# Performance work log

Hardware: AMD Instinct MI355X
Metric: run time of the kernel (lower is better)

Reference implementation:

```python
import jax, jax.numpy as jnp
import numpy as np

P = 8      # input_path_dim
D = 64     # cde_state_dim
W = 16     # signature_window_size
OUT = 32   # output_path_dim
II, JJ = np.triu_indices(P, k=1)   # Lyndon words of length 2: (i, j) with i < j
L = P + II.shape[0]                # logsig size at depth 2 = 8 + 28 = 36


def lipswish(x):
    return 0.909 * jax.nn.silu(x)


def setup_inputs() -> dict:
    key = jax.random.key(0)
    ks = jax.random.split(key, 16)
    s = lambda *sh: 1.0 / np.sqrt(sh[-1])
    inp = {
        "control_values": jax.random.normal(ks[0], (32, 257, P), dtype=jnp.float32),
        # initial-condition MLP: P -> 128 -> 128 -> D, lipswish activations
        "ic_w1": jax.random.normal(ks[1], (128, P)) * s(128, P),
        "ic_b1": jnp.zeros((128,)),
        "ic_w2": jax.random.normal(ks[2], (128, 128)) * s(128, 128),
        "ic_b2": jnp.zeros((128,)),
        "ic_w3": jax.random.normal(ks[3], (D, 128)) * s(D, 128),
        "ic_b3": jnp.zeros((D,)),
        # vector-field MLP: D -> 128 -> 128 -> P*D, lipswish, final tanh
        "vf_w1": jax.random.normal(ks[4], (128, D)) * s(128, D),
        "vf_b1": jnp.zeros((128,)),
        "vf_w2": jax.random.normal(ks[5], (128, 128)) * s(128, 128),
        "vf_b2": jnp.zeros((128,)),
        "vf_w3": jax.random.normal(ks[6], (P * D, 128)) * s(P * D, 128),
        "vf_b3": jnp.zeros((P * D,)),
        # readout: D -> OUT
        "ro_w": jax.random.normal(ks[7], (OUT, D)) * s(OUT, D),
        "ro_b": jnp.zeros((OUT,)),
    }
    return {k: v.astype(jnp.float32) for k, v in inp.items()}


def _windowed_logsigs(x):
    """Depth-2 Lyndon log-signatures of piecewise-linear path x: (length, P) -> (n_windows, L)."""
    dx = jnp.diff(x, axis=0).reshape(-1, W, P)          # (nw, W, P) increments
    lev1 = dx.sum(axis=1)                               # (nw, P)
    pre = jnp.cumsum(dx, axis=1) - dx                   # X_k - X_0 within window
    s = jnp.einsum("wki,wkj->wij", pre, dx)             # iterated-integral cross terms
    area = 0.5 * (s - jnp.swapaxes(s, 1, 2))            # Levy area, antisymmetric
    lev2 = area[:, II, JJ]                              # Lyndon coords i<j: (nw, P*(P-1)/2)
    return jnp.concatenate([lev1, lev2], axis=1)        # (nw, L)


def reference(control_values, ic_w1, ic_b1, ic_w2, ic_b2, ic_w3, ic_b3,
              vf_w1, vf_b1, vf_w2, vf_b2, vf_w3, vf_b3, ro_w, ro_b):
    def ic_mlp(x):
        h = lipswish(ic_w1 @ x + ic_b1)
        h = lipswish(ic_w2 @ h + ic_b2)
        return ic_w3 @ h + ic_b3

    def vf(y):  # all P vector fields stacked: (P, D)
        h = lipswish(vf_w1 @ y + vf_b1)
        h = lipswish(vf_w2 @ h + vf_b2)
        return jnp.tanh(vf_w3 @ h + vf_b3).reshape(P, D)

    def vf_matrix(y):
        # Euclidean manifold: retract / project_to_tangent are identity.
        F = vf(y)                        # (P, D)  level-1 columns f_i(y)
        J = jax.jacfwd(vf)(y)            # (P, D, D) Jacobians df_a/dy
        M = jnp.einsum("ade,be->abd", J, F)     # M[a,b] = J_a @ f_b
        lev2 = M[JJ, II] - M[II, JJ]     # [f_i, f_j](y) = Jf_j f_i - Jf_i f_j
        return jnp.concatenate([F, lev2], axis=0).T  # (D, L)

    def solve_one(x):  # x: (length, P)
        logsigs = _windowed_logsigs(x)   # (nw, L)
        y0 = ic_mlp(x[0])
        def step(y, v):                  # one RK4 step per window (log-ODE)
            g = lambda z: vf_matrix(z) @ v
            k1 = g(y); k2 = g(y + 0.5 * k1); k3 = g(y + 0.5 * k2); k4 = g(y + k3)
            y2 = y + (k1 + 2.0 * k2 + 2.0 * k3 + k4) / 6.0
            return y2, y2
        _, ys = jax.lax.scan(step, y0, logsigs)
        hidden = jnp.concatenate([y0[None], ys], axis=0)   # (nw+1, D) evolving output
        return hidden @ ro_w.T + ro_b                      # readout, identity retract

    return jax.vmap(solve_one)(control_values)             # (B, nw+1, OUT)
```

## Files before the change

### kernel.cpp

```cpp
#include <hip/hip_runtime.h>
#include <math.h>

#define NT 1024

#define D_YCUR 0
#define D_KACC 64
#define D_T3   128
#define D_VSIG 640
#define D_HID  1216
#define D_X0   2304
#define D_TOTAL 2312

#define F_YB 0
#define F_H1 96
#define F_D1 256
#define F_H2 384
#define F_D2 544
#define F_FB 672
#define F_WM 1184
#define F_U1 1696
#define F_U2 2976
#define F_CM 4256
#define F_TOTAL 4320

static __device__ __forceinline__ double lipswish_d(double z, double* d) {
    double s = 1.0 / (1.0 + exp(-z));
    *d = 0.909 * s * (1.0 + z * (1.0 - s));
    return 0.909 * z * s;
}
static __device__ __forceinline__ float lipswish_f(float z, float* d) {
    float s = 1.0f / (1.0f + expf(-z));
    *d = 0.909f * s * (1.0f + z * (1.0f - s));
    return 0.909f * z * s;
}

template<int CTRL>
static __device__ __forceinline__ float dpp_mov_f(float v) {
    int xx = __builtin_amdgcn_update_dpp(0, __float_as_int(v), CTRL, 0xF, 0xF, false);
    return __int_as_float(xx);
}
static __device__ __forceinline__ float red8f(float v) {
    v += dpp_mov_f<0xB1>(v);
    v += dpp_mov_f<0x4E>(v);
    v += dpp_mov_f<0x141>(v);
    return v;
}
static __device__ __forceinline__ float red16f(float v) {
    v += dpp_mov_f<0xB1>(v);
    v += dpp_mov_f<0x4E>(v);
    v += dpp_mov_f<0x141>(v);
    v += dpp_mov_f<0x128>(v);
    return v;
}
static __device__ __forceinline__ float red4f(float v) {
    v += dpp_mov_f<0xB1>(v);
    v += dpp_mov_f<0x4E>(v);
    return v;
}
static __device__ __forceinline__ float red2f(float v) {
    return v + dpp_mov_f<0xB1>(v);
}

extern "C" __global__ void __launch_bounds__(NT, 1)
ncde_solve(const float* __restrict__ x,
           const float* __restrict__ ic_w1, const float* __restrict__ ic_b1,
           const float* __restrict__ ic_w2, const float* __restrict__ ic_b2,
           const float* __restrict__ ic_w3, const float* __restrict__ ic_b3,
           const float* __restrict__ vf_w1, const float* __restrict__ vf_b1,
           const float* __restrict__ vf_w2, const float* __restrict__ vf_b2,
           const float* __restrict__ vf_w3, const float* __restrict__ vf_b3,
           const float* __restrict__ ro_w,  const float* __restrict__ ro_b,
           float* __restrict__ out)
{
    __shared__ double smd[D_TOTAL];
    __shared__ __align__(16) float smf[F_TOTAL];

    const int t = threadIdx.x;
    const int b = blockIdx.x;
    const float* xb = x + (size_t)b * (257 * 8);

    const int o8 = t >> 3, p8 = t & 7;
    const int o16 = t >> 4, p16 = t & 15;
    const int m = t >> 2, q = t & 3;
    const int aT = t >> 7;

    float w1f[8];
    {
        const float4* s4 = reinterpret_cast<const float4*>(vf_w1 + o8 * 64 + 8 * p8);
        float4 v0 = s4[0], v1 = s4[1];
        w1f[0] = v0.x; w1f[1] = v0.y; w1f[2] = v0.z; w1f[3] = v0.w;
        w1f[4] = v1.x; w1f[5] = v1.y; w1f[6] = v1.z; w1f[7] = v1.w;
    }
    float w2f[16];
    {
        const float4* s4 = reinterpret_cast<const float4*>(vf_w2 + o8 * 128 + 16 * p8);
        #pragma unroll
        for (int jj = 0; jj < 4; ++jj) {
            float4 v = s4[jj];
            w2f[4 * jj] = v.x; w2f[4 * jj + 1] = v.y;
            w2f[4 * jj + 2] = v.z; w2f[4 * jj + 3] = v.w;
        }
    }
    float w1u[2][4];
    {
        float4 a = *reinterpret_cast<const float4*>(vf_w1 + o16 * 64 + 4 * p16);
        float4 c = *reinterpret_cast<const float4*>(vf_w1 + (o16 + 64) * 64 + 4 * p16);
        w1u[0][0] = a.x; w1u[0][1] = a.y; w1u[0][2] = a.z; w1u[0][3] = a.w;
        w1u[1][0] = c.x; w1u[1][1] = c.y; w1u[1][2] = c.z; w1u[1][3] = c.w;
    }
    float w2u[2][8];
    {
        const float4* sa = reinterpret_cast<const float4*>(vf_w2 + o16 * 128 + 8 * p16);
        const float4* sb = reinterpret_cast<const float4*>(vf_w2 + (o16 + 64) * 128 + 8 * p16);
        float4 a0 = sa[0], a1 = sa[1], c0 = sb[0], c1 = sb[1];
        w2u[0][0] = a0.x; w2u[0][1] = a0.y; w2u[0][2] = a0.z; w2u[0][3] = a0.w;
        w2u[0][4] = a1.x; w2u[0][5] = a1.y; w2u[0][6] = a1.z; w2u[0][7] = a1.w;
        w2u[1][0] = c0.x; w2u[1][1] = c0.y; w2u[1][2] = c0.z; w2u[1][3] = c0.w;
        w2u[1][4] = c1.x; w2u[1][5] = c1.y; w2u[1][6] = c1.z; w2u[1][7] = c1.w;
    }
    float w3a[32], w3b[32];
    {
        const float4* sa = reinterpret_cast<const float4*>(vf_w3 + (size_t)(2 * m) * 128 + 32 * q);
        const float4* sb = reinterpret_cast<const float4*>(vf_w3 + (size_t)(2 * m + 1) * 128 + 32 * q);
        #pragma unroll
        for (int jj = 0; jj < 8; ++jj) {
            float4 va = sa[jj], vb = sb[jj];
            w3a[4 * jj] = va.x; w3a[4 * jj + 1] = va.y; w3a[4 * jj + 2] = va.z; w3a[4 * jj + 3] = va.w;
            w3b[4 * jj] = vb.x; w3b[4 * jj + 1] = vb.y; w3b[4 * jj + 2] = vb.z; w3b[4 * jj + 3] = vb.w;
        }
    }
    const float b1o = vf_b1[o8];
    const float b2o = vf_b2[o8];
    const float b3a = vf_b3[2 * m];
    const float b3b = vf_b3[2 * m + 1];

    if (t < 8) smd[D_X0 + t] = (double)xb[t];
    if (t < 16) {
        const float* xr = xb + t * 16 * 8;
        double cum[8], area[28], prev[8];
        #pragma unroll
        for (int i = 0; i < 8; ++i) { cum[i] = 0.0; prev[i] = (double)xr[i]; }
        #pragma unroll
        for (int u = 0; u < 28; ++u) area[u] = 0.0;
        for (int k = 1; k <= 16; ++k) {
            double dx[8];
            #pragma unroll
            for (int i = 0; i < 8; ++i) {
                double c = (double)xr[k * 8 + i];
                dx[i] = c - prev[i];
                prev[i] = c;
            }
            #pragma unroll
            for (int i = 0; i < 7; ++i) {
                #pragma unroll
                for (int j = i + 1; j < 8; ++j) {
                    int u = 7 * i - (i * (i - 1)) / 2 + (j - i - 1);
                    area[u] += 0.5 * (cum[i] * dx[j] - cum[j] * dx[i]);
                }
            }
            #pragma unroll
            for (int i = 0; i < 8; ++i) cum[i] += dx[i];
        }
        #pragma unroll
        for (int i = 0; i < 8; ++i) smd[D_VSIG + t * 36 + i] = cum[i];
        #pragma unroll
        for (int u = 0; u < 28; ++u) smd[D_VSIG + t * 36 + 8 + u] = area[u];
    }
    __syncthreads();

    if (t < 128) {
        double acc = (double)ic_b1[t];
        #pragma unroll
        for (int e = 0; e < 8; ++e) acc += (double)ic_w1[t * 8 + e] * smd[D_X0 + e];
        double d;
        smd[D_T3 + t] = lipswish_d(acc, &d);
    }
    __syncthreads();
    if (t < 128) {
        const float4* wr = reinterpret_cast<const float4*>(ic_w2 + t * 128);
        double a0 = 0.0, a1 = 0.0, a2 = 0.0, a3 = 0.0;
        #pragma unroll
        for (int k = 0; k < 32; ++k) {
            float4 wv = wr[k];
            double2 h0 = *reinterpret_cast<const double2*>(&smd[D_T3 + 4 * k]);
            double2 h1 = *reinterpret_cast<const double2*>(&smd[D_T3 + 4 * k + 2]);
            a0 += (double)wv.x * h0.x; a1 += (double)wv.y * h0.y;
            a2 += (double)wv.z * h1.x; a3 += (double)wv.w * h1.y;
        }
        double d;
        smd[D_T3 + 128 + t] = lipswish_d((double)ic_b2[t] + (a0 + a2) + (a1 + a3), &d);
    }
    __syncthreads();
    if (t < 64) {
        const float4* wr = reinterpret_cast<const float4*>(ic_w3 + t * 128);
        double a0 = 0.0, a1 = 0.0, a2 = 0.0, a3 = 0.0;
        #pragma unroll
        for (int k = 0; k < 32; ++k) {
            float4 wv = wr[k];
            double2 h0 = *reinterpret_cast<const double2*>(&smd[D_T3 + 128 + 4 * k]);
            double2 h1 = *reinterpret_cast<const double2*>(&smd[D_T3 + 128 + 4 * k + 2]);
            a0 += (double)wv.x * h0.x; a1 += (double)wv.y * h0.y;
            a2 += (double)wv.z * h1.x; a3 += (double)wv.w * h1.y;
        }
        double y0 = (double)ic_b3[t] + (a0 + a2) + (a1 + a3);
        smd[D_YCUR + t] = y0;
        smd[D_HID + t]  = y0;
        smf[F_YB + t + 4 * (t >> 3)] = (float)y0;
        int a = t >> 3, bb = t & 7;
        double cv = 0.0;
        if (a != bb) {
            int i = a < bb ? a : bb;
            int j = a < bb ? bb : a;
            int pidx = 7 * i - (i * (i - 1)) / 2 + (j - i - 1);
            double vv = smd[D_VSIG + 8 + pidx];
            cv = (a > bb) ? vv : -vv;
        }
        smf[F_CM + t] = (float)cv;
    }
    __syncthreads();

    for (int w = 0; w < 16; ++w) {
        for (int stage = 0; stage < 4; ++stage) {
            {
                float4 y0 = *reinterpret_cast<const float4*>(&smf[F_YB + 12 * p8]);
                float4 y1 = *reinterpret_cast<const float4*>(&smf[F_YB + 12 * p8 + 4]);
                float acc = w1f[0] * y0.x + w1f[1] * y0.y + w1f[2] * y0.z + w1f[3] * y0.w
                          + w1f[4] * y1.x + w1f[5] * y1.y + w1f[6] * y1.z + w1f[7] * y1.w;
                acc = red8f(acc);
                if (p8 == 0) {
                    float d;
                    smf[F_H1 + o8 + 4 * (o8 >> 4)] = lipswish_f(acc + b1o, &d);
                    smf[F_D1 + o8] = d;
                }
            }
            __syncthreads();
            {
                const float4* hv = reinterpret_cast<const float4*>(&smf[F_H1 + 20 * p8]);
                float4 h0 = hv[0], h1 = hv[1], h2 = hv[2], h3 = hv[3];
                float a0 = w2f[0] * h0.x + w2f[1] * h0.y + w2f[2] * h0.z + w2f[3] * h0.w
                         + w2f[4] * h1.x + w2f[5] * h1.y + w2f[6] * h1.z + w2f[7] * h1.w;
                float a1 = w2f[8] * h2.x + w2f[9] * h2.y + w2f[10] * h2.z + w2f[11] * h2.w
                         + w2f[12] * h3.x + w2f[13] * h3.y + w2f[14] * h3.z + w2f[15] * h3.w;
                float acc = red8f(a0 + a1);
                if (p8 == 0) {
                    float d;
                    smf[F_H2 + o8 + 4 * (o8 >> 4)] = lipswish_f(acc + b2o, &d);
                    smf[F_D2 + o8] = d;
                }
            }
            __syncthreads();
            float F0 = 0.0f, F1 = 0.0f;
            {
                float a0 = 0.0f, a1 = 0.0f;
                #pragma unroll
                for (int jj = 0; jj < 8; ++jj) {
                    float4 hv = *reinterpret_cast<const float4*>(
                        &smf[F_H2 + 40 * q + 4 * jj + 4 * (jj >> 2)]);
                    a0 += w3a[4 * jj] * hv.x + w3a[4 * jj + 1] * hv.y
                        + w3a[4 * jj + 2] * hv.z + w3a[4 * jj + 3] * hv.w;
                    a1 += w3b[4 * jj] * hv.x + w3b[4 * jj + 1] * hv.y
                        + w3b[4 * jj + 2] * hv.z + w3b[4 * jj + 3] * hv.w;
                }
                a0 = red4f(a0);
                a1 = red4f(a1);
                if (q == 0) {
                    F0 = tanhf(a0 + b3a);
                    F1 = tanhf(a1 + b3b);
                    float2 fv; fv.x = F0; fv.y = F1;
                    *reinterpret_cast<float2*>(&smf[F_FB + 2 * m]) = fv;
                }
            }
            __syncthreads();
            if (t < 128) {
                int a = t >> 4, eq = t & 15;
                float cm[8];
                #pragma unroll
                for (int bb = 0; bb < 8; ++bb) cm[bb] = smf[F_CM + a * 8 + bb];
                float4 s; s.x = 0.0f; s.y = 0.0f; s.z = 0.0f; s.w = 0.0f;
                #pragma unroll
                for (int bb = 0; bb < 8; ++bb) {
                    float4 fv = *reinterpret_cast<const float4*>(&smf[F_FB + bb * 64 + 4 * eq]);
                    s.x += cm[bb] * fv.x; s.y += cm[bb] * fv.y;
                    s.z += cm[bb] * fv.z; s.w += cm[bb] * fv.w;
                }
                *reinterpret_cast<float4*>(&smf[F_WM + a * 64 + 4 * eq]) = s;
            }
            __syncthreads();
            {
                float d1a = smf[F_D1 + o16], d1b = smf[F_D1 + o16 + 64];
                int ob = F_U1 + o16 + 4 * (o16 >> 4);
                #pragma unroll
                for (int half = 0; half < 2; ++half) {
                    float a0[4], a1[4];
                    #pragma unroll
                    for (int ai = 0; ai < 4; ++ai) {
                        int a = 4 * half + ai;
                        float4 mv = *reinterpret_cast<const float4*>(&smf[F_WM + a * 64 + 4 * p16]);
                        a0[ai] = w1u[0][0] * mv.x + w1u[0][1] * mv.y + w1u[0][2] * mv.z + w1u[0][3] * mv.w;
                        a1[ai] = w1u[1][0] * mv.x + w1u[1][1] * mv.y + w1u[1][2] * mv.z + w1u[1][3] * mv.w;
                    }
                    #pragma unroll
                    for (int ai = 0; ai < 4; ++ai) {
                        a0[ai] = red16f(a0[ai]);
                        a1[ai] = red16f(a1[ai]);
                    }
                    if (p16 == 0) {
                        #pragma unroll
                        for (int ai = 0; ai < 4; ++ai) {
                            int a = 4 * half + ai;
                            smf[ob + a * 160]      = a0[ai] * d1a;
                            smf[ob + a * 160 + 80] = a1[ai] * d1b;
                        }
                    }
                }
            }
            __syncthreads();
            {
                float d2a = smf[F_D2 + o16], d2b = smf[F_D2 + o16 + 64];
                int ib = 8 * p16 + 4 * (p16 >> 1);
                int ob = F_U2 + o16 + 4 * (o16 >> 4);
                #pragma unroll
                for (int half = 0; half < 2; ++half) {
                    float a0[4], a1[4];
                    #pragma unroll
                    for (int ai = 0; ai < 4; ++ai) {
                        int a = 4 * half + ai;
                        float4 u0 = *reinterpret_cast<const float4*>(&smf[F_U1 + a * 160 + ib]);
                        float4 u1 = *reinterpret_cast<const float4*>(&smf[F_U1 + a * 160 + ib + 4]);
                        a0[ai] = w2u[0][0] * u0.x + w2u[0][1] * u0.y + w2u[0][2] * u0.z + w2u[0][3] * u0.w
                               + w2u[0][4] * u1.x + w2u[0][5] * u1.y + w2u[0][6] * u1.z + w2u[0][7] * u1.w;
                        a1[ai] = w2u[1][0] * u0.x + w2u[1][1] * u0.y + w2u[1][2] * u0.z + w2u[1][3] * u0.w
                               + w2u[1][4] * u1.x + w2u[1][5] * u1.y + w2u[1][6] * u1.z + w2u[1][7] * u1.w;
                    }
                    #pragma unroll
                    for (int ai = 0; ai < 4; ++ai) {
                        a0[ai] = red16f(a0[ai]);
                        a1[ai] = red16f(a1[ai]);
                    }
                    if (p16 == 0) {
                        #pragma unroll
                        for (int ai = 0; ai < 4; ++ai) {
                            int a = 4 * half + ai;
                            smf[ob + a * 160]      = a0[ai] * d2a;
                            smf[ob + a * 160 + 80] = a1[ai] * d2b;
                        }
                    }
                }
            }
            __syncthreads();
            {
                float a0 = 0.0f, a1 = 0.0f;
                #pragma unroll
                for (int jj = 0; jj < 8; ++jj) {
                    float4 uv = *reinterpret_cast<const float4*>(
                        &smf[F_U2 + aT * 160 + 40 * q + 4 * jj + 4 * (jj >> 2)]);
                    a0 += w3a[4 * jj] * uv.x + w3a[4 * jj + 1] * uv.y
                        + w3a[4 * jj + 2] * uv.z + w3a[4 * jj + 3] * uv.w;
                    a1 += w3b[4 * jj] * uv.x + w3b[4 * jj + 1] * uv.y
                        + w3b[4 * jj + 2] * uv.z + w3b[4 * jj + 3] * uv.w;
                }
                a0 = red4f(a0);
                a1 = red4f(a1);
                if (q == 0) {
                    double va = smd[D_VSIG + w * 36 + aT];
                    double2 tv;
                    tv.x = va * (double)F0 + (1.0 - (double)F0 * F0) * (double)a0;
                    tv.y = va * (double)F1 + (1.0 - (double)F1 * F1) * (double)a1;
                    *reinterpret_cast<double2*>(&smd[D_T3 + 2 * m]) = tv;
                }
            }
            __syncthreads();
            if (t < 64) {
                double g = 0.0;
                #pragma unroll
                for (int a = 0; a < 8; ++a) g += smd[D_T3 + a * 64 + t];
                double y = smd[D_YCUR + t];
                int yp = F_YB + t + 4 * (t >> 3);
                if (stage == 0)      { smd[D_KACC + t] = g;        smf[yp] = (float)(y + 0.5 * g); }
                else if (stage == 1) { smd[D_KACC + t] += 2.0 * g; smf[yp] = (float)(y + 0.5 * g); }
                else if (stage == 2) { smd[D_KACC + t] += 2.0 * g; smf[yp] = (float)(y + g); }
                else {
                    double yn = y + (smd[D_KACC + t] + g) * (1.0 / 6.0);
                    smd[D_YCUR + t] = yn;
                    smf[yp] = (float)yn;
                    smd[D_HID + (w + 1) * 64 + t] = yn;
                }
            } else if (t < 128 && stage == 3 && w < 15) {
                int idx = t - 64;
                int a = idx >> 3, bb = idx & 7;
                double cv = 0.0;
                if (a != bb) {
                    int i = a < bb ? a : bb;
                    int j = a < bb ? bb : a;
                    int pidx = 7 * i - (i * (i - 1)) / 2 + (j - i - 1);
                    double vv = smd[D_VSIG + (w + 1) * 36 + 8 + pidx];
                    cv = (a > bb) ? vv : -vv;
                }
                smf[F_CM + idx] = (float)cv;
            }
            __syncthreads();
        }
    }

    for (int idx = t; idx < 544; idx += NT) {
        int s = idx >> 5, oo = idx & 31;
        double acc = (double)ro_b[oo];
        const float* wr = ro_w + oo * 64;
        const double* hr = &smd[D_HID + s * 64];
        #pragma unroll
        for (int d = 0; d < 64; ++d) acc += (double)wr[d] * hr[d];
        out[(size_t)b * 544 + idx] = (float)acc;
    }
}

extern "C" void kernel_launch(void* const* d_in, const int* in_sizes, int n_in,
                              void* d_out, int out_size, void* d_ws, size_t ws_size,
                              hipStream_t stream) {
    const float* x     = (const float*)d_in[0];
    const float* ic_w1 = (const float*)d_in[1];
    const float* ic_b1 = (const float*)d_in[2];
    const float* ic_w2 = (const float*)d_in[3];
    const float* ic_b2 = (const float*)d_in[4];
    const float* ic_w3 = (const float*)d_in[5];
    const float* ic_b3 = (const float*)d_in[6];
    const float* vf_w1 = (const float*)d_in[7];
    const float* vf_b1 = (const float*)d_in[8];
    const float* vf_w2 = (const float*)d_in[9];
    const float* vf_b2 = (const float*)d_in[10];
    const float* vf_w3 = (const float*)d_in[11];
    const float* vf_b3 = (const float*)d_in[12];
    const float* ro_w  = (const float*)d_in[13];
    const float* ro_b  = (const float*)d_in[14];
    float* out = (float*)d_out;

    int B = in_sizes[0] / (257 * 8);
    hipLaunchKernelGGL(ncde_solve, dim3(B), dim3(NT), 0, stream,
                       x, ic_w1, ic_b1, ic_w2, ic_b2, ic_w3, ic_b3,
                       vf_w1, vf_b1, vf_w2, vf_b2, vf_w3, vf_b3, ro_w, ro_b, out);
}
```

Baseline: 622.6 us.

## Process two batch sequences per block to amortize barriers and weight loads

Each block now integrates two independent sequences, interleaving their work between the same barriers, with shared memory doubled and moved to dynamic allocation. The grid is halved. The intent is to amortize barrier latency and register-resident weights over two sequences and expose more ILP. The cost is fewer blocks on a machine that is already underfilled, plus doubled serial work per block.

```diff
diff --git a/kernel.cpp b/kernel.cpp
--- a/kernel.cpp
+++ b/kernel.cpp
@@ -23,6 +23,8 @@
 #define F_CM 4256
 #define F_TOTAL 4320
 
+#define SMEM_BYTES (2 * D_TOTAL * 8 + 2 * F_TOTAL * 4)
+
 static __device__ __forceinline__ double lipswish_d(double z, double* d) {
     double s = 1.0 / (1.0 + exp(-z));
     *d = 0.909 * s * (1.0 + z * (1.0 - s));
@@ -56,9 +58,6 @@
     v += dpp_mov_f<0xB1>(v);
     v += dpp_mov_f<0x4E>(v);
     return v;
-}
-static __device__ __forceinline__ float red2f(float v) {
-    return v + dpp_mov_f<0xB1>(v);
 }
 
 extern "C" __global__ void __launch_bounds__(NT, 1)
@@ -70,14 +69,17 @@
            const float* __restrict__ vf_w2, const float* __restrict__ vf_b2,
            const float* __restrict__ vf_w3, const float* __restrict__ vf_b3,
            const float* __restrict__ ro_w,  const float* __restrict__ ro_b,
-           float* __restrict__ out)
+           float* __restrict__ out, int B)
 {
-    __shared__ double smd[D_TOTAL];
-    __shared__ __align__(16) float smf[F_TOTAL];
+    extern __shared__ char smraw[];
+    double* smdA = reinterpret_cast<double*>(smraw);
+    float*  smfA = reinterpret_cast<float*>(smdA + 2 * D_TOTAL);
 
     const int t = threadIdx.x;
-    const int b = blockIdx.x;
-    const float* xb = x + (size_t)b * (257 * 8);
+    int gs0 = 2 * blockIdx.x,     gs1 = 2 * blockIdx.x + 1;
+    const bool live1 = gs1 < B;
+    if (!live1) gs1 = B - 1;
+    const int gseq[2] = {gs0, gs1};
 
     const int o8 = t >> 3, p8 = t & 7;
     const int o16 = t >> 4, p16 = t & 15;
@@ -134,108 +136,131 @@
     const float b3a = vf_b3[2 * m];
     const float b3b = vf_b3[2 * m + 1];
 
-    if (t < 8) smd[D_X0 + t] = (double)xb[t];
-    if (t < 16) {
-        const float* xr = xb + t * 16 * 8;
-        double cum[8], area[28], prev[8];
-        #pragma unroll
-        for (int i = 0; i < 8; ++i) { cum[i] = 0.0; prev[i] = (double)xr[i]; }
-        #pragma unroll
-        for (int u = 0; u < 28; ++u) area[u] = 0.0;
-        for (int k = 1; k <= 16; ++k) {
-            double dx[8];
-            #pragma unroll
-            for (int i = 0; i < 8; ++i) {
-                double c = (double)xr[k * 8 + i];
-                dx[i] = c - prev[i];
-                prev[i] = c;
-            }
-            #pragma unroll
-            for (int i = 0; i < 7; ++i) {
-                #pragma unroll
-                for (int j = i + 1; j < 8; ++j) {
-                    int u = 7 * i - (i * (i - 1)) / 2 + (j - i - 1);
-                    area[u] += 0.5 * (cum[i] * dx[j] - cum[j] * dx[i]);
-                }
-            }
-            #pragma unroll
-            for (int i = 0; i < 8; ++i) cum[i] += dx[i];
-        }
-        #pragma unroll
-        for (int i = 0; i < 8; ++i) smd[D_VSIG + t * 36 + i] = cum[i];
-        #pragma unroll
-        for (int u = 0; u < 28; ++u) smd[D_VSIG + t * 36 + 8 + u] = area[u];
+    #pragma unroll
+    for (int s = 0; s < 2; ++s) {
+        double* sd = smdA + s * D_TOTAL;
+        const float* xb = x + (size_t)gseq[s] * (257 * 8);
+        if (t < 8) sd[D_X0 + t] = (double)xb[t];
+        if (t < 16) {
+            const float* xr = xb + t * 16 * 8;
+            double cum[8], area[28], prev[8];
+            #pragma unroll
+            for (int i = 0; i < 8; ++i) { cum[i] = 0.0; prev[i] = (double)xr[i]; }
+            #pragma unroll
+            for (int u = 0; u < 28; ++u) area[u] = 0.0;
+            for (int k = 1; k <= 16; ++k) {
+                double dx[8];
+                #pragma unroll
+                for (int i = 0; i < 8; ++i) {
+                    double c = (double)xr[k * 8 + i];
+                    dx[i] = c - prev[i];
+                    prev[i] = c;
+                }
+                #pragma unroll
+                for (int i = 0; i < 7; ++i) {
+                    #pragma unroll
+                    for (int j = i + 1; j < 8; ++j) {
+                        int u = 7 * i - (i * (i - 1)) / 2 + (j - i - 1);
+                        area[u] += 0.5 * (cum[i] * dx[j] - cum[j] * dx[i]);
+                    }
+                }
+                #pragma unroll
+                for (int i = 0; i < 8; ++i) cum[i] += dx[i];
+            }
+            #pragma unroll
+            for (int i = 0; i < 8; ++i) sd[D_VSIG + t * 36 + i] = cum[i];
+            #pragma unroll
+            for (int u = 0; u < 28; ++u) sd[D_VSIG + t * 36 + 8 + u] = area[u];
+        }
     }
     __syncthreads();
 
-    if (t < 128) {
-        double acc = (double)ic_b1[t];
-        #pragma unroll
-        for (int e = 0; e < 8; ++e) acc += (double)ic_w1[t * 8 + e] * smd[D_X0 + e];
-        double d;
-        smd[D_T3 + t] = lipswish_d(acc, &d);
+    #pragma unroll
+    for (int s = 0; s < 2; ++s) {
+        double* sd = smdA + s * D_TOTAL;
+        if (t < 128) {
+            double acc = (double)ic_b1[t];
+            #pragma unroll
+            for (int e = 0; e < 8; ++e) acc += (double)ic_w1[t * 8 + e] * sd[D_X0 + e];
+            double d;
+            sd[D_T3 + t] = lipswish_d(acc, &d);
+        }
     }
     __syncthreads();
-    if (t < 128) {
-        const float4* wr = reinterpret_cast<const float4*>(ic_w2 + t * 128);
-        double a0 = 0.0, a1 = 0.0, a2 = 0.0, a3 = 0.0;
-        #pragma unroll
-        for (int k = 0; k < 32; ++k) {
-            float4 wv = wr[k];
-            double2 h0 = *reinterpret_cast<const double2*>(&smd[D_T3 + 4 * k]);
-            double2 h1 = *reinterpret_cast<const double2*>(&smd[D_T3 + 4 * k + 2]);
-            a0 += (double)wv.x * h0.x; a1 += (double)wv.y * h0.y;
-            a2 += (double)wv.z * h1.x; a3 += (double)wv.w * h1.y;
-        }
-        double d;
-        smd[D_T3 + 128 + t] = lipswish_d((double)ic_b2[t] + (a0 + a2) + (a1 + a3), &d);
+    #pragma unroll
+    for (int s = 0; s < 2; ++s) {
+        double* sd = smdA + s * D_TOTAL;
+        if (t < 128) {
+            const float4* wr = reinterpret_cast<const float4*>(ic_w2 + t * 128);
+            double a0 = 0.0, a1 = 0.0, a2 = 0.0, a3 = 0.0;
+            #pragma unroll
+            for (int k = 0; k < 32; ++k) {
+                float4 wv = wr[k];
+                double2 h0 = *reinterpret_cast<const double2*>(&sd[D_T3 + 4 * k]);
+                double2 h1 = *reinterpret_cast<const double2*>(&sd[D_T3 + 4 * k + 2]);
+                a0 += (double)wv.x * h0.x; a1 += (double)wv.y * h0.y;
+                a2 += (double)wv.z * h1.x; a3 += (double)wv.w * h1.y;
+            }
+            double d;
+            sd[D_T3 + 128 + t] = lipswish_d((double)ic_b2[t] + (a0 + a2) + (a1 + a3), &d);
+        }
     }
     __syncthreads();
-    if (t < 64) {
-        const float4* wr = reinterpret_cast<const float4*>(ic_w3 + t * 128);
-        double a0 = 0.0, a1 = 0.0, a2 = 0.0, a3 = 0.0;
-        #pragma unroll
-        for (int k = 0; k < 32; ++k) {
-            float4 wv = wr[k];
-            double2 h0 = *reinterpret_cast<const double2*>(&smd[D_T3 + 128 + 4 * k]);
-            double2 h1 = *reinterpret_cast<const double2*>(&smd[D_T3 + 128 + 4 * k + 2]);
-            a0 += (double)wv.x * h0.x; a1 += (double)wv.y * h0.y;
-            a2 += (double)wv.z * h1.x; a3 += (double)wv.w * h1.y;
-        }
-        double y0 = (double)ic_b3[t] + (a0 + a2) + (a1 + a3);
-        smd[D_YCUR + t] = y0;
-        smd[D_HID + t]  = y0;
-        smf[F_YB + t + 4 * (t >> 3)] = (float)y0;
-        int a = t >> 3, bb = t & 7;
-        double cv = 0.0;
-        if (a != bb) {
-            int i = a < bb ? a : bb;
-            int j = a < bb ? bb : a;
-            int pidx = 7 * i - (i * (i - 1)) / 2 + (j - i - 1);
-            double vv = smd[D_VSIG + 8 + pidx];
-            cv = (a > bb) ? vv : -vv;
-        }
-        smf[F_CM + t] = (float)cv;
+    #pragma unroll
+    for (int s = 0; s < 2; ++s) {
+        double* sd = smdA + s * D_TOTAL;
+        float*  sf = smfA + s * F_TOTAL;
+        if (t < 64) {
+            const float4* wr = reinterpret_cast<const float4*>(ic_w3 + t * 128);
+            double a0 = 0.0, a1 = 0.0, a2 = 0.0, a3 = 0.0;
+            #pragma unroll
+            for (int k = 0; k < 32; ++k) {
+                float4 wv = wr[k];
+                double2 h0 = *reinterpret_cast<const double2*>(&sd[D_T3 + 128 + 4 * k]);
+                double2 h1 = *reinterpret_cast<const double2*>(&sd[D_T3 + 128 + 4 * k + 2]);
+                a0 += (double)wv.x * h0.x; a1 += (double)wv.y * h0.y;
+                a2 += (double)wv.z * h1.x; a3 += (double)wv.w * h1.y;
+            }
+            double y0 = (double)ic_b3[t] + (a0 + a2) + (a1 + a3);
+            sd[D_YCUR + t] = y0;
+            sd[D_HID + t]  = y0;
+            sf[F_YB + t + 4 * (t >> 3)] = (float)y0;
+            int a = t >> 3, bb = t & 7;
+            double cv = 0.0;
+            if (a != bb) {
+                int i = a < bb ? a : bb;
+                int j = a < bb ? bb : a;
+                int pidx = 7 * i - (i * (i - 1)) / 2 + (j - i - 1);
+                double vv = sd[D_VSIG + 8 + pidx];
+                cv = (a > bb) ? vv : -vv;
+            }
+            sf[F_CM + t] = (float)cv;
+        }
     }
     __syncthreads();
 
     for (int w = 0; w < 16; ++w) {
         for (int stage = 0; stage < 4; ++stage) {
-            {
-                float4 y0 = *reinterpret_cast<const float4*>(&smf[F_YB + 12 * p8]);
-                float4 y1 = *reinterpret_cast<const float4*>(&smf[F_YB + 12 * p8 + 4]);
+            float F0s[2], F1s[2];
+            #pragma unroll
+            for (int s = 0; s < 2; ++s) {
+                float* sf = smfA + s * F_TOTAL;
+                float4 y0 = *reinterpret_cast<const float4*>(&sf[F_YB + 12 * p8]);
+                float4 y1 = *reinterpret_cast<const float4*>(&sf[F_YB + 12 * p8 + 4]);
                 float acc = w1f[0] * y0.x + w1f[1] * y0.y + w1f[2] * y0.z + w1f[3] * y0.w
                           + w1f[4] * y1.x + w1f[5] * y1.y + w1f[6] * y1.z + w1f[7] * y1.w;
                 acc = red8f(acc);
                 if (p8 == 0) {
                     float d;
-                    smf[F_H1 + o8 + 4 * (o8 >> 4)] = lipswish_f(acc + b1o, &d);
-                    smf[F_D1 + o8] = d;
-                }
-            }
-            __syncthreads();
-            {
-                const float4* hv = reinterpret_cast<const float4*>(&smf[F_H1 + 20 * p8]);
+                    sf[F_H1 + o8 + 4 * (o8 >> 4)] = lipswish_f(acc + b1o, &d);
+                    sf[F_D1 + o8] = d;
+                }
+            }
+            __syncthreads();
+            #pragma unroll
+            for (int s = 0; s < 2; ++s) {
+                float* sf = smfA + s * F_TOTAL;
+                const float4* hv = reinterpret_cast<const float4*>(&sf[F_H1 + 20 * p8]);
                 float4 h0 = hv[0], h1 = hv[1], h2 = hv[2], h3 = hv[3];
                 float a0 = w2f[0] * h0.x + w2f[1] * h0.y + w2f[2] * h0.z + w2f[3] * h0.w
                          + w2f[4] * h1.x + w2f[5] * h1.y + w2f[6] * h1.z + w2f[7] * h1.w;
@@ -244,18 +269,19 @@
                 float acc = red8f(a0 + a1);
                 if (p8 == 0) {
                     float d;
-                    smf[F_H2 + o8 + 4 * (o8 >> 4)] = lipswish_f(acc + b2o, &d);
-                    smf[F_D2 + o8] = d;
-                }
-            }
-            __syncthreads();
-            float F0 = 0.0f, F1 = 0.0f;
-            {
+                    sf[F_H2 + o8 + 4 * (o8 >> 4)] = lipswish_f(acc + b2o, &d);
+                    sf[F_D2 + o8] = d;
+                }
+            }
+            __syncthreads();
+            #pragma unroll
+            for (int s = 0; s < 2; ++s) {
+                float* sf = smfA + s * F_TOTAL;
                 float a0 = 0.0f, a1 = 0.0f;
                 #pragma unroll
                 for (int jj = 0; jj < 8; ++jj) {
                     float4 hv = *reinterpret_cast<const float4*>(
-                        &smf[F_H2 + 40 * q + 4 * jj + 4 * (jj >> 2)]);
+                        &sf[F_H2 + 40 * q + 4 * jj + 4 * (jj >> 2)]);
                     a0 += w3a[4 * jj] * hv.x + w3a[4 * jj + 1] * hv.y
                         + w3a[4 * jj + 2] * hv.z + w3a[4 * jj + 3] * hv.w;
                     a1 += w3b[4 * jj] * hv.x + w3b[4 * jj + 1] * hv.y
@@ -263,31 +289,38 @@
                 }
                 a0 = red4f(a0);
                 a1 = red4f(a1);
+                F0s[s] = 0.0f; F1s[s] = 0.0f;
                 if (q == 0) {
-                    F0 = tanhf(a0 + b3a);
-                    F1 = tanhf(a1 + b3b);
-                    float2 fv; fv.x = F0; fv.y = F1;
-                    *reinterpret_cast<float2*>(&smf[F_FB + 2 * m]) = fv;
-                }
-            }
-            __syncthreads();
-            if (t < 128) {
-                int a = t >> 4, eq = t & 15;
-                float cm[8];
-                #pragma unroll
-                for (int bb = 0; bb < 8; ++bb) cm[bb] = smf[F_CM + a * 8 + bb];
-                float4 s; s.x = 0.0f; s.y = 0.0f; s.z = 0.0f; s.w = 0.0f;
-                #pragma unroll
-                for (int bb = 0; bb < 8; ++bb) {
-                    float4 fv = *reinterpret_cast<const float4*>(&smf[F_FB + bb * 64 + 4 * eq]);
-                    s.x += cm[bb] * fv.x; s.y += cm[bb] * fv.y;
-                    s.z += cm[bb] * fv.z; s.w += cm[bb] * fv.w;
-                }
-                *reinterpret_cast<float4*>(&smf[F_WM + a * 64 + 4 * eq]) = s;
-            }
-            __syncthreads();
-            {
-                float d1a = smf[F_D1 + o16], d1b = smf[F_D1 + o16 + 64];
+                    F0s[s] = tanhf(a0 + b3a);
+                    F1s[s] = tanhf(a1 + b3b);
+                    float2 fv; fv.x = F0s[s]; fv.y = F1s[s];
+                    *reinterpret_cast<float2*>(&sf[F_FB + 2 * m]) = fv;
+                }
+            }
+            __syncthreads();
+            #pragma unroll
+            for (int s = 0; s < 2; ++s) {
+                float* sf = smfA + s * F_TOTAL;
+                if (t < 128) {
+                    int a = t >> 4, eq = t & 15;
+                    float cm[8];
+                    #pragma unroll
+                    for (int bb = 0; bb < 8; ++bb) cm[bb] = sf[F_CM + a * 8 + bb];
+                    float4 sv; sv.x = 0.0f; sv.y = 0.0f; sv.z = 0.0f; sv.w = 0.0f;
+                    #pragma unroll
+                    for (int bb = 0; bb < 8; ++bb) {
+                        float4 fv = *reinterpret_cast<const float4*>(&sf[F_FB + bb * 64 + 4 * eq]);
+                        sv.x += cm[bb] * fv.x; sv.y += cm[bb] * fv.y;
+                        sv.z += cm[bb] * fv.z; sv.w += cm[bb] * fv.w;
+                    }
+                    *reinterpret_cast<float4*>(&sf[F_WM + a * 64 + 4 * eq]) = sv;
+                }
+            }
+            __syncthreads();
+            #pragma unroll
+            for (int s = 0; s < 2; ++s) {
+                float* sf = smfA + s * F_TOTAL;
+                float d1a = sf[F_D1 + o16], d1b = sf[F_D1 + o16 + 64];
                 int ob = F_U1 + o16 + 4 * (o16 >> 4);
                 #pragma unroll
                 for (int half = 0; half < 2; ++half) {
@@ -295,7 +328,7 @@
                     #pragma unroll
                     for (int ai = 0; ai < 4; ++ai) {
                         int a = 4 * half + ai;
-                        float4 mv = *reinterpret_cast<const float4*>(&smf[F_WM + a * 64 + 4 * p16]);
+                        float4 mv = *reinterpret_cast<const float4*>(&sf[F_WM + a * 64 + 4 * p16]);
                         a0[ai] = w1u[0][0] * mv.x + w1u[0][1] * mv.y + w1u[0][2] * mv.z + w1u[0][3] * mv.w;
                         a1[ai] = w1u[1][0] * mv.x + w1u[1][1] * mv.y + w1u[1][2] * mv.z + w1u[1][3] * mv.w;
                     }
@@ -308,15 +341,17 @@
                         #pragma unroll
                         for (int ai = 0; ai < 4; ++ai) {
                             int a = 4 * half + ai;
-                            smf[ob + a * 160]      = a0[ai] * d1a;
-                            smf[ob + a * 160 + 80] = a1[ai] * d1b;
+                            sf[ob + a * 160]      = a0[ai] * d1a;
+                            sf[ob + a * 160 + 80] = a1[ai] * d1b;
                         }
                     }
                 }
             }
             __syncthreads();
-            {
-                float d2a = smf[F_D2 + o16], d2b = smf[F_D2 + o16 + 64];
+            #pragma unroll
+            for (int s = 0; s < 2; ++s) {
+                float* sf = smfA + s * F_TOTAL;
+                float d2a = sf[F_D2 + o16], d2b = sf[F_D2 + o16 + 64];
                 int ib = 8 * p16 + 4 * (p16 >> 1);
                 int ob = F_U2 + o16 + 4 * (o16 >> 4);
                 #pragma unroll
@@ -325,8 +360,8 @@
                     #pragma unroll
                     for (int ai = 0; ai < 4; ++ai) {
                         int a = 4 * half + ai;
-                        float4 u0 = *reinterpret_cast<const float4*>(&smf[F_U1 + a * 160 + ib]);
-                        float4 u1 = *reinterpret_cast<const float4*>(&smf[F_U1 + a * 160 + ib + 4]);
+                        float4 u0 = *reinterpret_cast<const float4*>(&sf[F_U1 + a * 160 + ib]);
+                        float4 u1 = *reinterpret_cast<const float4*>(&sf[F_U1 + a * 160 + ib + 4]);
                         a0[ai] = w2u[0][0] * u0.x + w2u[0][1] * u0.y + w2u[0][2] * u0.z + w2u[0][3] * u0.w
                                + w2u[0][4] * u1.x + w2u[0][5] * u1.y + w2u[0][6] * u1.z + w2u[0][7] * u1.w;
                         a1[ai] = w2u[1][0] * u0.x + w2u[1][1] * u0.y + w2u[1][2] * u0.z + w2u[1][3] * u0.w
@@ -341,19 +376,22 @@
                         #pragma unroll
                         for (int ai = 0; ai < 4; ++ai) {
                             int a = 4 * half + ai;
-                            smf[ob + a * 160]      = a0[ai] * d2a;
-                            smf[ob + a * 160 + 80] = a1[ai] * d2b;
+                            sf[ob + a * 160]      = a0[ai] * d2a;
+                            sf[ob + a * 160 + 80] = a1[ai] * d2b;
                         }
                     }
                 }
             }
             __syncthreads();
-            {
+            #pragma unroll
+            for (int s = 0; s < 2; ++s) {
+                double* sd = smdA + s * D_TOTAL;
+                float*  sf = smfA + s * F_TOTAL;
                 float a0 = 0.0f, a1 = 0.0f;
                 #pragma unroll
                 for (int jj = 0; jj < 8; ++jj) {
                     float4 uv = *reinterpret_cast<const float4*>(
-                        &smf[F_U2 + aT * 160 + 40 * q + 4 * jj + 4 * (jj >> 2)]);
+                        &sf[F_U2 + aT * 160 + 40 * q + 4 * jj + 4 * (jj >> 2)]);
                     a0 += w3a[4 * jj] * uv.x + w3a[4 * jj + 1] * uv.y
                         + w3a[4 * jj + 2] * uv.z + w3a[4 * jj + 3] * uv.w;
                     a1 += w3b[4 * jj] * uv.x + w3b[4 * jj + 1] * uv.y
@@ -362,54 +400,65 @@
                 a0 = red4f(a0);
                 a1 = red4f(a1);
                 if (q == 0) {
-                    double va = smd[D_VSIG + w * 36 + aT];
+                    double va = sd[D_VSIG + w * 36 + aT];
+                    double F0 = F0s[s], F1 = F1s[s];
                     double2 tv;
-                    tv.x = va * (double)F0 + (1.0 - (double)F0 * F0) * (double)a0;
-                    tv.y = va * (double)F1 + (1.0 - (double)F1 * F1) * (double)a1;
-                    *reinterpret_cast<double2*>(&smd[D_T3 + 2 * m]) = tv;
-                }
-            }
-            __syncthreads();
-            if (t < 64) {
-                double g = 0.0;
-                #pragma unroll
-                for (int a = 0; a < 8; ++a) g += smd[D_T3 + a * 64 + t];
-                double y = smd[D_YCUR + t];
-                int yp = F_YB + t + 4 * (t >> 3);
-                if (stage == 0)      { smd[D_KACC + t] = g;        smf[yp] = (float)(y + 0.5 * g); }
-                else if (stage == 1) { smd[D_KACC + t] += 2.0 * g; smf[yp] = (float)(y + 0.5 * g); }
-                else if (stage == 2) { smd[D_KACC + t] += 2.0 * g; smf[yp] = (float)(y + g); }
-                else {
-                    double yn = y + (smd[D_KACC + t] + g) * (1.0 / 6.0);
-                    smd[D_YCUR + t] = yn;
-                    smf[yp] = (float)yn;
-                    smd[D_HID + (w + 1) * 64 + t] = yn;
-                }
-            } else if (t < 128 && stage == 3 && w < 15) {
-                int idx = t - 64;
-                int a = idx >> 3, bb = idx & 7;
-                double cv = 0.0;
-                if (a != bb) {
-                    int i = a < bb ? a : bb;
-                    int j = a < bb ? bb : a;
-                    int pidx = 7 * i - (i * (i - 1)) / 2 + (j - i - 1);
-                    double vv = smd[D_VSIG + (w + 1) * 36 + 8 + pidx];
-                    cv = (a > bb) ? vv : -vv;
-                }
-                smf[F_CM + idx] = (float)cv;
-            }
-            __syncthreads();
-        }
-    }
-
-    for (int idx = t; idx < 544; idx += NT) {
-        int s = idx >> 5, oo = idx & 31;
-        double acc = (double)ro_b[oo];
-        const float* wr = ro_w + oo * 64;
-        const double* hr = &smd[D_HID + s * 64];
-        #pragma unroll
-        for (int d = 0; d < 64; ++d) acc += (double)wr[d] * hr[d];
-        out[(size_t)b * 544 + idx] = (float)acc;
+                    tv.x = va * F0 + (1.0 - F0 * F0) * (double)a0;
+                    tv.y = va * F1 + (1.0 - F1 * F1) * (double)a1;
+                    *reinterpret_cast<double2*>(&sd[D_T3 + 2 * m]) = tv;
+                }
+            }
+            __syncthreads();
+            #pragma unroll
+            for (int s = 0; s < 2; ++s) {
+                double* sd = smdA + s * D_TOTAL;
+                float*  sf = smfA + s * F_TOTAL;
+                if (t < 64) {
+                    double g = 0.0;
+                    #pragma unroll
+                    for (int a = 0; a < 8; ++a) g += sd[D_T3 + a * 64 + t];
+                    double y = sd[D_YCUR + t];
+                    int yp = F_YB + t + 4 * (t >> 3);
+                    if (stage == 0)      { sd[D_KACC + t] = g;        sf[yp] = (float)(y + 0.5 * g); }
+                    else if (stage == 1) { sd[D_KACC + t] += 2.0 * g; sf[yp] = (float)(y + 0.5 * g); }
+                    else if (stage == 2) { sd[D_KACC + t] += 2.0 * g; sf[yp] = (float)(y + g); }
+                    else {
+                        double yn = y + (sd[D_KACC + t] + g) * (1.0 / 6.0);
+                        sd[D_YCUR + t] = yn;
+                        sf[yp] = (float)yn;
+                        sd[D_HID + (w + 1) * 64 + t] = yn;
+                    }
+                } else if (t < 128 && stage == 3 && w < 15) {
+                    int idx = t - 64;
+                    int a = idx >> 3, bb = idx & 7;
+                    double cv = 0.0;
+                    if (a != bb) {
+                        int i = a < bb ? a : bb;
+                        int j = a < bb ? bb : a;
+                        int pidx = 7 * i - (i * (i - 1)) / 2 + (j - i - 1);
+                        double vv = sd[D_VSIG + (w + 1) * 36 + 8 + pidx];
+                        cv = (a > bb) ? vv : -vv;
+                    }
+                    sf[F_CM + idx] = (float)cv;
+                }
+            }
+            __syncthreads();
+        }
+    }
+
+    #pragma unroll
+    for (int s = 0; s < 2; ++s) {
+        if (s == 1 && !live1) break;
+        double* sd = smdA + s * D_TOTAL;
+        for (int idx = t; idx < 544; idx += NT) {
+            int sr = idx >> 5, oo = idx & 31;
+            double acc = (double)ro_b[oo];
+            const float* wr = ro_w + oo * 64;
+            const double* hr = &sd[D_HID + sr * 64];
+            #pragma unroll
+            for (int d = 0; d < 64; ++d) acc += (double)wr[d] * hr[d];
+            out[(size_t)gseq[s] * 544 + idx] = (float)acc;
+        }
     }
 }
 
@@ -434,7 +483,10 @@
     float* out = (float*)d_out;
 
     int B = in_sizes[0] / (257 * 8);
-    hipLaunchKernelGGL(ncde_solve, dim3(B), dim3(NT), 0, stream,
+    int grid = (B + 1) / 2;
+    hipFuncSetAttribute(reinterpret_cast<const void*>(ncde_solve),
+                        hipFuncAttributeMaxDynamicSharedMemorySize, SMEM_BYTES);
+    hipLaunchKernelGGL(ncde_solve, dim3(grid), dim3(NT), SMEM_BYTES, stream,
                        x, ic_w1, ic_b1, ic_w2, ic_b2, ic_w3, ic_b3,
-                       vf_w1, vf_b1, vf_w2, vf_b2, vf_w3, vf_b3, ro_w, ro_b, out);
-}
+                       vf_w1, vf_b1, vf_w2, vf_b2, vf_w3, vf_b3, ro_w, ro_b, out, B);
+}
```

New measurement: 1.971 ms. 3.17x slower.
